# Kernel tuning notes

Measured on AMD Instinct MI355X. Metric: run time of the kernel, lower is better.

Reference implementation:

```python
import jax, jax.numpy as jnp
import numpy as np
import math

D_INNER = 512
D_STATE = 16
DT_RANK = 32
B_SZ = 2
L_SEQ = 4096


def setup_inputs() -> dict:
    key = jax.random.key(0)
    ks = jax.random.split(key, 6)
    x = jax.random.normal(ks[0], (B_SZ, L_SEQ, D_INNER), dtype=jnp.float32)
    # parameters (match torch init semantics closely enough for a numeric baseline)
    A = jnp.arange(1, D_STATE + 1, dtype=jnp.float32)
    A_log = jnp.broadcast_to(jnp.log(A)[None, :], (D_INNER, D_STATE)).copy()
    D_param = jnp.ones((D_INNER,), dtype=jnp.float32)
    # x_proj: Linear(d_inner -> dt_rank + 2*d_state), no bias
    W_xproj = jax.random.normal(ks[1], (DT_RANK + 2 * D_STATE, D_INNER), dtype=jnp.float32) / np.sqrt(D_INNER)
    # dt_proj: Linear(dt_rank -> d_inner) with special bias init
    W_dt = jax.random.normal(ks[2], (D_INNER, DT_RANK), dtype=jnp.float32) / np.sqrt(DT_RANK)
    dt_init = jnp.exp(jax.random.uniform(ks[3], (D_INNER,)) * (math.log(0.1) - math.log(0.001)) + math.log(0.001))
    b_dt = jnp.log(jnp.exp(dt_init) - 1.0)
    alpha = jnp.asarray(0.6, dtype=jnp.float32)
    beta_logit = jnp.asarray(math.log(0.99 / (1.0 - 0.99 + 1e-08)), dtype=jnp.float32)
    return {"x": x, "A_log": A_log, "D_param": D_param, "W_xproj": W_xproj,
            "W_dt": W_dt, "b_dt": b_dt, "alpha": alpha, "beta_logit": beta_logit}


def _momentum_ssm(x, A_log, D_param, W_xproj, W_dt, b_dt, alpha, beta_logit):
    # x: (B, L, D)
    proj = jnp.einsum('bld,pd->blp', x, W_xproj)            # (B, L, r+2N)
    dt_in = proj[..., :DT_RANK]
    Bp = proj[..., DT_RANK:DT_RANK + D_STATE]                # (B, L, N)
    Cp = proj[..., DT_RANK + D_STATE:]                       # (B, L, N)
    dt = jax.nn.softplus(jnp.einsum('blr,dr->bld', dt_in, W_dt) + b_dt)  # (B, L, D)
    A = -jnp.exp(A_log)                                      # (D, N)
    A_bar = jnp.exp(dt[..., None] * A[None, None])           # (B, L, D, N)
    # fused B_bar * x_t: dt * Bp * x
    inp = dt[..., None] * Bp[:, :, None, :] * x[..., None]   # (B, L, D, N)
    beta = jax.nn.sigmoid(beta_logit)

    # scan over time; carry (h, v): (B, D, N)
    h0 = jnp.zeros((x.shape[0], D_INNER, D_STATE), dtype=x.dtype)
    v0 = jnp.zeros_like(h0)

    def step(carry, ts):
        h, v = carry
        a_t, inp_t, c_t = ts                                 # (B,D,N), (B,D,N), (B,N)
        v = beta * v + alpha * inp_t
        h = a_t * h + v
        y = jnp.einsum('bdn,bn->bd', h, c_t)
        return (h, v), y

    xs = (jnp.moveaxis(A_bar, 1, 0), jnp.moveaxis(inp, 1, 0), jnp.moveaxis(Cp, 1, 0))
    _, ys = jax.lax.scan(step, (h0, v0), xs)                 # ys: (L, B, D)
    y = jnp.moveaxis(ys, 0, 1)                               # (B, L, D)
    return y + D_param * x


def reference(x, A_log, D_param, W_xproj, W_dt, b_dt, alpha, beta_logit):
    return _momentum_ssm(x, A_log, D_param, W_xproj, W_dt, b_dt, alpha, beta_logit)
```

## Files before the change

kernel.cpp:

```cpp
#include <hip/hip_runtime.h>


#define D_IN 512
#define D_ST 16
#define DTR  32
#define BSZ  2
#define LSEQ 4096
#define PDIM 64
#define NCH  256
#define LCH  (LSEQ / NCH)
#define LOG2E 1.44269504f
#define LN2   0.69314718f

typedef __attribute__((ext_vector_type(8))) short short8;
typedef __attribute__((ext_vector_type(4))) float f32x4;
typedef _Float16 f16;
typedef __attribute__((ext_vector_type(8))) _Float16 f16x8;

__device__ inline float fast_exp2(float x) { return __builtin_amdgcn_exp2f(x); }
__device__ inline float fast_log2(float x) { return __builtin_amdgcn_logf(x); }

__device__ inline unsigned short bf16_rne(float f) {
  unsigned b = __float_as_uint(f);
  return (unsigned short)((b + 0x7fffu + ((b >> 16) & 1u)) >> 16);
}

__device__ inline void cvt8(const float4 u, const float4 v, short8& hi, short8& lo) {
  float f[8] = {u.x, u.y, u.z, u.w, v.x, v.y, v.z, v.w};
#pragma unroll
  for (int i = 0; i < 8; ++i) {
    unsigned short h = bf16_rne(f[i]);
    hi[i] = (short)h;
    float r = f[i] - __uint_as_float((unsigned)h << 16);
    lo[i] = (short)bf16_rne(r);
  }
}

__device__ inline void st8h(f16* p, const float* s) {
  f16 t[8];
#pragma unroll
  for (int i = 0; i < 8; ++i) t[i] = (f16)s[i];
  *(f16x8*)p = *(f16x8*)&t[0];
}
__device__ inline void ld16h(const f16* p, float* d) {
  f16x8 a = *(const f16x8*)p;
  f16x8 b = *(const f16x8*)(p + 8);
#pragma unroll
  for (int i = 0; i < 8; ++i) { d[i] = (float)a[i]; d[8 + i] = (float)b[i]; }
}

__device__ inline bool loadA2(const float* A_log, int d, float* A2) {
  const float4* ap = (const float4*)(A_log + (size_t)d * D_ST);
#pragma unroll
  for (int i = 0; i < 4; ++i) {
    float4 a4 = ap[i];
    A2[4 * i + 0] = -__expf(a4.x) * LOG2E;
    A2[4 * i + 1] = -__expf(a4.y) * LOG2E;
    A2[4 * i + 2] = -__expf(a4.z) * LOG2E;
    A2[4 * i + 3] = -__expf(a4.w) * LOG2E;
  }
  bool pw = true;
#pragma unroll
  for (int n = 1; n < 16; ++n) {
    float ref = (float)(n + 1) * A2[0];
    pw = pw && (fabsf(A2[n] - ref) <= 2e-5f * fabsf(ref));
  }
  return pw;
}

__global__ __launch_bounds__(256) void k_wprep(const float* __restrict__ W,
                                               short* __restrict__ Whi,
                                               short* __restrict__ Wlo) {
  const int i = (blockIdx.x * 256 + threadIdx.x) * 4;
  float4 w = *(const float4*)(W + i);
  float f[4] = {w.x, w.y, w.z, w.w};
  unsigned short h[4], lo[4];
#pragma unroll
  for (int j = 0; j < 4; ++j) {
    h[j] = bf16_rne(f[j]);
    float r = f[j] - __uint_as_float((unsigned)h[j] << 16);
    lo[j] = bf16_rne(r);
  }
  *(uint2*)(Whi + i) = make_uint2(h[0] | ((unsigned)h[1] << 16), h[2] | ((unsigned)h[3] << 16));
  *(uint2*)(Wlo + i) = make_uint2(lo[0] | ((unsigned)lo[1] << 16), lo[2] | ((unsigned)lo[3] << 16));
}

#define MM3(ACC, AH, AL, BH, BL)                                        \
  ACC = __builtin_amdgcn_mfma_f32_16x16x32_bf16(AL, BH, ACC, 0, 0, 0);  \
  ACC = __builtin_amdgcn_mfma_f32_16x16x32_bf16(AH, BL, ACC, 0, 0, 0);  \
  ACC = __builtin_amdgcn_mfma_f32_16x16x32_bf16(AH, BH, ACC, 0, 0, 0);

#define LOADB(P, S)                                   \
  {                                                   \
    const int kb = ((S) & 15) * 32;                   \
    P##h0 = *(const short8*)(bh + kb);                \
    P##h1 = *(const short8*)(bh + 8192 + kb);         \
    P##h2 = *(const short8*)(bh + 16384 + kb);        \
    P##h3 = *(const short8*)(bh + 24576 + kb);        \
    P##l0 = *(const short8*)(bl + kb);                \
    P##l1 = *(const short8*)(bl + 8192 + kb);         \
    P##l2 = *(const short8*)(bl + 16384 + kb);        \
    P##l3 = *(const short8*)(bl + 24576 + kb);        \
  }

#define LOADA(Aa, Ab, S)                              \
  {                                                   \
    const int ka = ((S) & 15) * 32;                   \
    Aa = *(const float4*)(xr + ka);                   \
    Ab = *(const float4*)(xr + ka + 4);               \
  }

#define SUBSTEP(Aa, Ab, P, SA, SB)                    \
  {                                                   \
    short8 ahi, alo;                                  \
    cvt8(Aa, Ab, ahi, alo);                           \
    MM3(acc0, ahi, alo, P##h0, P##l0);                \
    MM3(acc1, ahi, alo, P##h1, P##l1);                \
    MM3(acc2, ahi, alo, P##h2, P##l2);                \
    MM3(acc3, ahi, alo, P##h3, P##l3);                \
    LOADB(P, SB);                                     \
    LOADA(Aa, Ab, SA);                                \
  }

__global__ __launch_bounds__(64) void k_proj(const float* __restrict__ x,
                                             const short* __restrict__ Whi,
                                             const short* __restrict__ Wlo,
                                             float* __restrict__ proj) {
  const int row0 = blockIdx.x * 16;
  const int l = threadIdx.x;
  const int m = l & 15;
  const int ko = (l >> 4) * 8;
  const float* xr = x + (size_t)(row0 + m) * D_IN + ko;
  const short* bh = Whi + (size_t)m * D_IN + ko;
  const short* bl = Wlo + (size_t)m * D_IN + ko;

  f32x4 acc0 = {0.f, 0.f, 0.f, 0.f}, acc1 = acc0, acc2 = acc0, acc3 = acc0;
  float4 A0a, A0b, A1a, A1b, A2a, A2b, A3a, A3b;
  short8 Xh0, Xh1, Xh2, Xh3, Xl0, Xl1, Xl2, Xl3;
  short8 Yh0, Yh1, Yh2, Yh3, Yl0, Yl1, Yl2, Yl3;
  LOADA(A0a, A0b, 0); LOADA(A1a, A1b, 1); LOADA(A2a, A2b, 2); LOADA(A3a, A3b, 3);
  LOADB(X, 0); LOADB(Y, 1);

#pragma unroll
  for (int it = 0; it < 4; ++it) {
    const int s = it * 4;
    SUBSTEP(A0a, A0b, X, s + 4, s + 2);
    SUBSTEP(A1a, A1b, Y, s + 5, s + 3);
    SUBSTEP(A2a, A2b, X, s + 6, s + 4);
    SUBSTEP(A3a, A3b, Y, s + 7, s + 5);
  }

  const int r0 = (l >> 4) * 4;
#pragma unroll
  for (int r = 0; r < 4; ++r) {
    float* pr = proj + (size_t)(row0 + r0 + r) * PDIM + m;
    pr[0] = acc0[r]; pr[16] = acc1[r]; pr[32] = acc2[r]; pr[48] = acc3[r];
  }
}


#define PWCHK(val, n)                                                        \
  pw = pw && (fabsf((val) - (float)((n) + 1) * a0) <=                        \
              2e-5f * fabsf((float)((n) + 1) * a0));

#define S1_LOOP                                                              \
  _Pragma("unroll")                                                          \
  for (int j = 0; j < LCH; ++j) {                                            \
    const float4* pj = (const float4*)&Ps[j][16 * hf];                       \
    float c0 = 0.f, c1 = 0.f, c2 = 0.f, c3 = 0.f;                            \
    _Pragma("unroll")                                                        \
    for (int k = 0; k < 4; ++k) {                                            \
      float4 p = pj[k];                                                      \
      c0 = fmaf(p.x, w4[k].x, c0);                                           \
      c1 = fmaf(p.y, w4[k].y, c1);                                           \
      c2 = fmaf(p.z, w4[k].z, c2);                                           \
      c3 = fmaf(p.w, w4[k].w, c3);                                           \
    }                                                                        \
    const float part = (c0 + c1) + (c2 + c3);                                \
    const float acc = part + __shfl_xor(part, 1, 64) + bb;                   \
    const float ee = fast_exp2(acc * LOG2E);                                 \
    const float dtc = (acc > 20.f) ? acc : LN2 * fast_log2(1.f + ee);        \
    if (hf == 0) dp[(size_t)j * D_IN] = (f16)dtc;                            \
    sd += dtc;                                                               \
    bpow *= beta;                                                            \
    const float xv = xs[j];                                                  \
    const float u = alpha * dtc * xv;                                        \
    float4 B0 = *(const float4*)&Ps[j][DTR + 8 * hf];                        \
    float4 B1 = *(const float4*)&Ps[j][DTR + 8 * hf + 4];                    \
    const float Bf[8] = {B0.x, B0.y, B0.z, B0.w, B1.x, B1.y, B1.z, B1.w};    \
    AR_INIT;                                                                 \
    _Pragma("unroll")                                                        \
    for (int k = 0; k < 8; ++k) {                                            \
      AR_STEP;                                                               \
      v8[k] = fmaf(beta, v8[k], u * Bf[k]);                                  \
      h8[k] = fmaf(ar, h8[k], v8[k]);                                        \
      cv8[k] = fmaf(ar, cv8[k], bpow);                                       \
    }                                                                        \
  }

__global__ __launch_bounds__(256) void k_scan1(const float* __restrict__ x,
                                               const float* __restrict__ proj,
                                               const float* __restrict__ A_log,
                                               const float* __restrict__ W_dt,
                                               const float* __restrict__ b_dt,
                                               const float* __restrict__ alpha_p,
                                               const float* __restrict__ beta_p,
                                               f16* __restrict__ hh,
                                               f16* __restrict__ vh,
                                               f16* __restrict__ cvv,
                                               float* __restrict__ sdt,
                                               f16* __restrict__ dth) {
  __shared__ float Ps[LCH][PDIM];
  const int c = blockIdx.x, b = blockIdx.z;
  const int hf = threadIdx.x & 1;
  const int d = blockIdx.y * 128 + (threadIdx.x >> 1);
  const int t0 = c * LCH;
  {
    const float4* src = (const float4*)(proj + ((size_t)b * LSEQ + t0) * PDIM);
    ((float4*)&Ps[0][0])[threadIdx.x] = src[threadIdx.x];
  }
  float xs[LCH];
  {
    const float* xp = x + ((size_t)b * LSEQ + t0) * D_IN + d;
#pragma unroll
    for (int j = 0; j < LCH; ++j) xs[j] = xp[(size_t)j * D_IN];
  }
  float4 w4[4];
  {
    const float4* wp = (const float4*)(W_dt + (size_t)d * DTR + 16 * hf);
#pragma unroll
    for (int i = 0; i < 4; ++i) w4[i] = wp[i];
  }
  const float bb = b_dt[d];
  const float alpha = alpha_p[0];
  const float beta = 1.f / (1.f + __expf(-beta_p[0]));

  float4 e0, e1, e2, e3;
  {
    const float4* ap = (const float4*)(A_log + (size_t)d * D_ST);
    float4 r0 = ap[0], r1 = ap[1], r2 = ap[2], r3 = ap[3];
    e0 = make_float4(-__expf(r0.x) * LOG2E, -__expf(r0.y) * LOG2E,
                     -__expf(r0.z) * LOG2E, -__expf(r0.w) * LOG2E);
    e1 = make_float4(-__expf(r1.x) * LOG2E, -__expf(r1.y) * LOG2E,
                     -__expf(r1.z) * LOG2E, -__expf(r1.w) * LOG2E);
    e2 = make_float4(-__expf(r2.x) * LOG2E, -__expf(r2.y) * LOG2E,
                     -__expf(r2.z) * LOG2E, -__expf(r2.w) * LOG2E);
    e3 = make_float4(-__expf(r3.x) * LOG2E, -__expf(r3.y) * LOG2E,
                     -__expf(r3.z) * LOG2E, -__expf(r3.w) * LOG2E);
  }
  const float a0 = e0.x;
  bool pw = true;
  PWCHK(e0.y, 1) PWCHK(e0.z, 2) PWCHK(e0.w, 3)
  PWCHK(e1.x, 4) PWCHK(e1.y, 5) PWCHK(e1.z, 6) PWCHK(e1.w, 7)
  PWCHK(e2.x, 8) PWCHK(e2.y, 9) PWCHK(e2.z, 10) PWCHK(e2.w, 11)
  PWCHK(e3.x, 12) PWCHK(e3.y, 13) PWCHK(e3.z, 14) PWCHK(e3.w, 15)
  float A2h[8];
  {
    float4 u0 = hf ? e2 : e0;
    float4 u1 = hf ? e3 : e1;
    A2h[0] = u0.x; A2h[1] = u0.y; A2h[2] = u0.z; A2h[3] = u0.w;
    A2h[4] = u1.x; A2h[5] = u1.y; A2h[6] = u1.z; A2h[7] = u1.w;
  }
  __syncthreads();

  f16* dp = dth + ((size_t)b * LSEQ + t0) * D_IN + d;
  float h8[8] = {}, v8[8] = {}, cv8[8] = {};
  float bpow = 1.f, sd = 0.f;

  if (pw) {
#define AR_INIT                                                   \
    const float r = fast_exp2(dtc * a0);                          \
    const float r2 = r * r;                                       \
    const float r4 = r2 * r2;                                     \
    float ar = hf ? r4 * r4 : 1.f
#define AR_STEP ar *= r
    S1_LOOP
#undef AR_INIT
#undef AR_STEP
  } else {
#define AR_INIT float ar
#define AR_STEP ar = fast_exp2(dtc * A2h[k])
    S1_LOOP
#undef AR_INIT
#undef AR_STEP
  }

  const size_t base = ((size_t)(b * NCH + c) * D_IN + d) * D_ST + hf * 8;
  st8h(hh + base, h8);
  st8h(vh + base, v8);
  st8h(cvv + base, cv8);
  if (hf == 0) sdt[(size_t)(b * NCH + c) * D_IN + d] = sd;
}

__global__ __launch_bounds__(64) void k_fix(f16* __restrict__ hh,
                                            f16* __restrict__ vh,
                                            const f16* __restrict__ cvv,
                                            const float* __restrict__ sdt,
                                            const float* __restrict__ A_log,
                                            const float* __restrict__ beta_p) {
  const int g = blockIdx.x * 64 + threadIdx.x;
  const int b = g >> 13;
  const int dn = g & 8191;
  const float beta = 1.f / (1.f + __expf(-beta_p[0]));
  const float A2 = -__expf(A_log[dn]) * LOG2E;
  float bL = beta;
#pragma unroll
  for (int i = 0; i < 4; ++i) bL *= bL;

  const size_t cs = (size_t)D_IN * D_ST;
  const size_t base = (size_t)b * NCH * cs + dn;
  const size_t sbase = (size_t)b * NCH * D_IN + (dn >> 4);

  float hg[8], vg[8], cg[8], sg[8];
#pragma unroll
  for (int i = 0; i < 8; ++i) {
    hg[i] = (float)hh[base + i * cs];
    vg[i] = (float)vh[base + i * cs];
    cg[i] = (float)cvv[base + i * cs];
    sg[i] = sdt[sbase + i * D_IN];
  }
  float H = 0.f, V = 0.f;
  for (int c0 = 0; c0 < NCH; c0 += 8) {
    const int cp = (c0 + 8) & (NCH - 1);
    float hn[8], vn[8], cn[8], sn[8];
#pragma unroll
    for (int i = 0; i < 8; ++i) {
      hn[i] = (float)hh[base + (size_t)(cp + i) * cs];
      vn[i] = (float)vh[base + (size_t)(cp + i) * cs];
      cn[i] = (float)cvv[base + (size_t)(cp + i) * cs];
      sn[i] = sdt[sbase + (size_t)(cp + i) * D_IN];
    }
#pragma unroll
    for (int i = 0; i < 8; ++i) {
      hh[base + (size_t)(c0 + i) * cs] = (f16)H;
      vh[base + (size_t)(c0 + i) * cs] = (f16)V;
      const float Pa = fast_exp2(sg[i] * A2);
      const float Hn = fmaf(Pa, H, fmaf(cg[i], V, hg[i]));
      V = fmaf(bL, V, vg[i]);
      H = Hn;
    }
#pragma unroll
    for (int i = 0; i < 8; ++i) { hg[i] = hn[i]; vg[i] = vn[i]; cg[i] = cn[i]; sg[i] = sn[i]; }
  }
}

#define S2_BODY(GET_A)                                        \
  _Pragma("unroll")                                           \
  for (int j = 0; j < LCH; ++j) {                             \
    const float dtc = dtv[j], xv = xs[j];                     \
    const float u = alpha * dtc * xv;                         \
    GET_A;                                                    \
    float4 Bq[8];                                             \
    _Pragma("unroll")                                         \
    for (int i = 0; i < 8; ++i) Bq[i] = ((const float4*)&Ps[j][DTR])[i]; \
    const float* Bf = (const float*)Bq;                       \
    float y0 = 0.f, y1 = 0.f, y2 = 0.f, y3 = 0.f;             \
    float ar = 1.f;                                           \
    _Pragma("unroll")                                         \
    for (int n = 0; n < 16; ++n) {                            \
      NEXT_A(ar, n);                                          \
      v[n] = fmaf(beta, v[n], u * Bf[n]);                     \
      h[n] = fmaf(ar, h[n], v[n]);                            \
      float hc = h[n] * Bf[16 + n];                           \
      if ((n & 3) == 0) y0 += hc;                             \
      else if ((n & 3) == 1) y1 += hc;                        \
      else if ((n & 3) == 2) y2 += hc;                        \
      else y3 += hc;                                          \
    }                                                         \
    op[(size_t)j * D_IN] = (y0 + y1) + (y2 + y3) + Dv * xv;   \
  }

__global__ __launch_bounds__(256) void k_scan2(const float* __restrict__ x,
                                               const f16* __restrict__ dth,
                                               const float* __restrict__ proj,
                                               const float* __restrict__ A_log,
                                               const float* __restrict__ D_param,
                                               const float* __restrict__ alpha_p,
                                               const float* __restrict__ beta_p,
                                               const f16* __restrict__ hh,
                                               const f16* __restrict__ vh,
                                               float* __restrict__ out) {
  __shared__ float Ps[LCH][PDIM];
  const int c = blockIdx.x, b = blockIdx.z;
  const int d = blockIdx.y * 256 + threadIdx.x;
  const int t0 = c * LCH;
  {
    const float4* src = (const float4*)(proj + ((size_t)b * LSEQ + t0) * PDIM);
    ((float4*)&Ps[0][0])[threadIdx.x] = src[threadIdx.x];
  }
  float xs[LCH], dtv[LCH];
  {
    const float* xp = x + ((size_t)b * LSEQ + t0) * D_IN + d;
    const f16* dp = dth + ((size_t)b * LSEQ + t0) * D_IN + d;
#pragma unroll
    for (int j = 0; j < LCH; ++j) xs[j] = xp[(size_t)j * D_IN];
#pragma unroll
    for (int j = 0; j < LCH; ++j) dtv[j] = (float)dp[(size_t)j * D_IN];
  }
  const float alpha = alpha_p[0];
  const float beta = 1.f / (1.f + __expf(-beta_p[0]));
  const float Dv = D_param[d];
  float A2[D_ST];
  const bool powA = loadA2(A_log, d, A2);
  const size_t ibase = ((size_t)(b * NCH + c) * D_IN + d) * D_ST;
  float h[16], v[16];
  ld16h(hh + ibase, h);
  ld16h(vh + ibase, v);
  __syncthreads();

  float* op = out + ((size_t)b * LSEQ + t0) * D_IN + d;
  if (powA) {
#define NEXT_A(ar, n) ar *= r
    S2_BODY(const float r = fast_exp2(dtc * A2[0]))
#undef NEXT_A
  } else {
#define NEXT_A(ar, n) ar = fast_exp2(dtc * A2[n])
    S2_BODY()
#undef NEXT_A
  }
}

extern "C" void kernel_launch(void* const* d_in, const int* in_sizes, int n_in,
                              void* d_out, int out_size, void* d_ws, size_t ws_size,
                              hipStream_t stream) {
  const float* x = (const float*)d_in[0];
  const float* A_log = (const float*)d_in[1];
  const float* D_param = (const float*)d_in[2];
  const float* W_xproj = (const float*)d_in[3];
  const float* W_dt = (const float*)d_in[4];
  const float* b_dt = (const float*)d_in[5];
  const float* alpha = (const float*)d_in[6];
  const float* beta_logit = (const float*)d_in[7];
  float* out = (float*)d_out;

  const size_t NST = (size_t)BSZ * NCH * D_IN * D_ST;
  float* ws = (float*)d_ws;
  float* proj = ws;
  float* sdt = proj + (size_t)BSZ * LSEQ * PDIM;
  f16* hh = (f16*)(sdt + (size_t)BSZ * NCH * D_IN);
  f16* vh = hh + NST;
  f16* cvv = vh + NST;
  f16* dth = cvv + NST;
  short* Whi = (short*)(dth + (size_t)BSZ * LSEQ * D_IN);
  short* Wlo = Whi + (size_t)PDIM * D_IN;

  k_wprep<<<dim3(PDIM * D_IN / 1024), dim3(256), 0, stream>>>(W_xproj, Whi, Wlo);
  k_proj<<<dim3(BSZ * LSEQ / 16), dim3(64), 0, stream>>>(x, Whi, Wlo, proj);
  k_scan1<<<dim3(NCH, D_IN / 128, BSZ), dim3(256), 0, stream>>>(
      x, proj, A_log, W_dt, b_dt, alpha, beta_logit, hh, vh, cvv, sdt, dth);
  k_fix<<<dim3(BSZ * D_IN * D_ST / 64), dim3(64), 0, stream>>>(hh, vh, cvv, sdt, A_log,
                                                               beta_logit);
  k_scan2<<<dim3(NCH, D_IN / 256, BSZ), dim3(256), 0, stream>>>(
      x, dth, proj, A_log, D_param, alpha, beta_logit, hh, vh, out);
}
```

Before: 176.0 us.

## Use one thread per channel in scan1 and read proj directly from global

The first scan kernel drops the two-threads-per-channel split (which needed a shuffle and half-state registers), so each thread now handles all 16 states and the full dt dot product. Both scan kernels stop staging proj rows through shared memory and a barrier, reading them straight from global memory, where all threads in a block share the same rows. The non-power fallback recomputes A on the fly through volatile loads instead of holding it in registers. Together this halves the scan1 grid and removes syncs, at the cost of more registers per thread and less parallelism.

```diff
diff --git a/kernel.cpp b/kernel.cpp
--- a/kernel.cpp
+++ b/kernel.cpp
@@ -36,11 +36,12 @@
   }
 }
 
-__device__ inline void st8h(f16* p, const float* s) {
-  f16 t[8];
-#pragma unroll
-  for (int i = 0; i < 8; ++i) t[i] = (f16)s[i];
+__device__ inline void st16h(f16* p, const float* s) {
+  f16 t[16];
+#pragma unroll
+  for (int i = 0; i < 16; ++i) t[i] = (f16)s[i];
   *(f16x8*)p = *(f16x8*)&t[0];
+  *(f16x8*)(p + 8) = *(f16x8*)&t[8];
 }
 __device__ inline void ld16h(const f16* p, float* d) {
   f16x8 a = *(const f16x8*)p;
@@ -49,22 +50,27 @@
   for (int i = 0; i < 8; ++i) { d[i] = (float)a[i]; d[8 + i] = (float)b[i]; }
 }
 
-__device__ inline bool loadA2(const float* A_log, int d, float* A2) {
+#define PWCHK(val, n)                                                        \
+  pw = pw && (fabsf((val) - (float)((n) + 1) * a0) <=                        \
+              2e-5f * fabsf((float)((n) + 1) * a0));
+
+__device__ inline bool detectA2(const float* __restrict__ A_log, int d, float& a0) {
   const float4* ap = (const float4*)(A_log + (size_t)d * D_ST);
-#pragma unroll
-  for (int i = 0; i < 4; ++i) {
-    float4 a4 = ap[i];
-    A2[4 * i + 0] = -__expf(a4.x) * LOG2E;
-    A2[4 * i + 1] = -__expf(a4.y) * LOG2E;
-    A2[4 * i + 2] = -__expf(a4.z) * LOG2E;
-    A2[4 * i + 3] = -__expf(a4.w) * LOG2E;
-  }
+  float4 r0 = ap[0], r1 = ap[1], r2 = ap[2], r3 = ap[3];
+  float4 e0 = make_float4(-__expf(r0.x) * LOG2E, -__expf(r0.y) * LOG2E,
+                          -__expf(r0.z) * LOG2E, -__expf(r0.w) * LOG2E);
+  float4 e1 = make_float4(-__expf(r1.x) * LOG2E, -__expf(r1.y) * LOG2E,
+                          -__expf(r1.z) * LOG2E, -__expf(r1.w) * LOG2E);
+  float4 e2 = make_float4(-__expf(r2.x) * LOG2E, -__expf(r2.y) * LOG2E,
+                          -__expf(r2.z) * LOG2E, -__expf(r2.w) * LOG2E);
+  float4 e3 = make_float4(-__expf(r3.x) * LOG2E, -__expf(r3.y) * LOG2E,
+                          -__expf(r3.z) * LOG2E, -__expf(r3.w) * LOG2E);
+  a0 = e0.x;
   bool pw = true;
-#pragma unroll
-  for (int n = 1; n < 16; ++n) {
-    float ref = (float)(n + 1) * A2[0];
-    pw = pw && (fabsf(A2[n] - ref) <= 2e-5f * fabsf(ref));
-  }
+  PWCHK(e0.y, 1) PWCHK(e0.z, 2) PWCHK(e0.w, 3)
+  PWCHK(e1.x, 4) PWCHK(e1.y, 5) PWCHK(e1.z, 6) PWCHK(e1.w, 7)
+  PWCHK(e2.x, 8) PWCHK(e2.y, 9) PWCHK(e2.z, 10) PWCHK(e2.w, 11)
+  PWCHK(e3.x, 12) PWCHK(e3.y, 13) PWCHK(e3.z, 14) PWCHK(e3.w, 15)
   return pw;
 }
 
@@ -158,43 +164,39 @@
   }
 }
 
-
-#define PWCHK(val, n)                                                        \
-  pw = pw && (fabsf((val) - (float)((n) + 1) * a0) <=                        \
-              2e-5f * fabsf((float)((n) + 1) * a0));
-
 #define S1_LOOP                                                              \
   _Pragma("unroll")                                                          \
   for (int j = 0; j < LCH; ++j) {                                            \
-    const float4* pj = (const float4*)&Ps[j][16 * hf];                       \
-    float c0 = 0.f, c1 = 0.f, c2 = 0.f, c3 = 0.f;                            \
-    _Pragma("unroll")                                                        \
-    for (int k = 0; k < 4; ++k) {                                            \
-      float4 p = pj[k];                                                      \
-      c0 = fmaf(p.x, w4[k].x, c0);                                           \
-      c1 = fmaf(p.y, w4[k].y, c1);                                           \
-      c2 = fmaf(p.z, w4[k].z, c2);                                           \
-      c3 = fmaf(p.w, w4[k].w, c3);                                           \
+    const float4* pj = (const float4*)(pb + j * PDIM);                       \
+    float4 pp[8];                                                            \
+    _Pragma("unroll")                                                        \
+    for (int k = 0; k < 8; ++k) pp[k] = pj[k];                               \
+    float c0 = bb, c1 = 0.f, c2 = 0.f, c3 = 0.f;                             \
+    _Pragma("unroll")                                                        \
+    for (int k = 0; k < 8; ++k) {                                            \
+      c0 = fmaf(pp[k].x, w4[k].x, c0);                                       \
+      c1 = fmaf(pp[k].y, w4[k].y, c1);                                       \
+      c2 = fmaf(pp[k].z, w4[k].z, c2);                                       \
+      c3 = fmaf(pp[k].w, w4[k].w, c3);                                       \
     }                                                                        \
-    const float part = (c0 + c1) + (c2 + c3);                                \
-    const float acc = part + __shfl_xor(part, 1, 64) + bb;                   \
+    const float acc = (c0 + c1) + (c2 + c3);                                 \
     const float ee = fast_exp2(acc * LOG2E);                                 \
     const float dtc = (acc > 20.f) ? acc : LN2 * fast_log2(1.f + ee);        \
-    if (hf == 0) dp[(size_t)j * D_IN] = (f16)dtc;                            \
+    dp[(size_t)j * D_IN] = (f16)dtc;                                         \
     sd += dtc;                                                               \
     bpow *= beta;                                                            \
-    const float xv = xs[j];                                                  \
-    const float u = alpha * dtc * xv;                                        \
-    float4 B0 = *(const float4*)&Ps[j][DTR + 8 * hf];                        \
-    float4 B1 = *(const float4*)&Ps[j][DTR + 8 * hf + 4];                    \
-    const float Bf[8] = {B0.x, B0.y, B0.z, B0.w, B1.x, B1.y, B1.z, B1.w};    \
+    const float u = alpha * dtc * xs[j];                                     \
+    float4 bq[4];                                                            \
+    _Pragma("unroll")                                                        \
+    for (int k = 0; k < 4; ++k) bq[k] = pj[8 + k];                           \
+    const float* Bf = (const float*)bq;                                      \
     AR_INIT;                                                                 \
     _Pragma("unroll")                                                        \
-    for (int k = 0; k < 8; ++k) {                                            \
+    for (int n = 0; n < 16; ++n) {                                           \
       AR_STEP;                                                               \
-      v8[k] = fmaf(beta, v8[k], u * Bf[k]);                                  \
-      h8[k] = fmaf(ar, h8[k], v8[k]);                                        \
-      cv8[k] = fmaf(ar, cv8[k], bpow);                                       \
+      v[n] = fmaf(beta, v[n], u * Bf[n]);                                    \
+      h[n] = fmaf(ar, h[n], v[n]);                                           \
+      cv[n] = fmaf(ar, cv[n], bpow);                                         \
     }                                                                        \
   }
 
@@ -210,86 +212,53 @@
                                                f16* __restrict__ cvv,
                                                float* __restrict__ sdt,
                                                f16* __restrict__ dth) {
-  __shared__ float Ps[LCH][PDIM];
   const int c = blockIdx.x, b = blockIdx.z;
-  const int hf = threadIdx.x & 1;
-  const int d = blockIdx.y * 128 + (threadIdx.x >> 1);
+  const int d = blockIdx.y * 256 + threadIdx.x;
   const int t0 = c * LCH;
-  {
-    const float4* src = (const float4*)(proj + ((size_t)b * LSEQ + t0) * PDIM);
-    ((float4*)&Ps[0][0])[threadIdx.x] = src[threadIdx.x];
-  }
+  const float* pb = proj + ((size_t)b * LSEQ + t0) * PDIM;
+
   float xs[LCH];
   {
     const float* xp = x + ((size_t)b * LSEQ + t0) * D_IN + d;
 #pragma unroll
     for (int j = 0; j < LCH; ++j) xs[j] = xp[(size_t)j * D_IN];
   }
-  float4 w4[4];
+  float4 w4[8];
   {
-    const float4* wp = (const float4*)(W_dt + (size_t)d * DTR + 16 * hf);
-#pragma unroll
-    for (int i = 0; i < 4; ++i) w4[i] = wp[i];
+    const float4* wp = (const float4*)(W_dt + (size_t)d * DTR);
+#pragma unroll
+    for (int i = 0; i < 8; ++i) w4[i] = wp[i];
   }
   const float bb = b_dt[d];
   const float alpha = alpha_p[0];
   const float beta = 1.f / (1.f + __expf(-beta_p[0]));
-
-  float4 e0, e1, e2, e3;
-  {
-    const float4* ap = (const float4*)(A_log + (size_t)d * D_ST);
-    float4 r0 = ap[0], r1 = ap[1], r2 = ap[2], r3 = ap[3];
-    e0 = make_float4(-__expf(r0.x) * LOG2E, -__expf(r0.y) * LOG2E,
-                     -__expf(r0.z) * LOG2E, -__expf(r0.w) * LOG2E);
-    e1 = make_float4(-__expf(r1.x) * LOG2E, -__expf(r1.y) * LOG2E,
-                     -__expf(r1.z) * LOG2E, -__expf(r1.w) * LOG2E);
-    e2 = make_float4(-__expf(r2.x) * LOG2E, -__expf(r2.y) * LOG2E,
-                     -__expf(r2.z) * LOG2E, -__expf(r2.w) * LOG2E);
-    e3 = make_float4(-__expf(r3.x) * LOG2E, -__expf(r3.y) * LOG2E,
-                     -__expf(r3.z) * LOG2E, -__expf(r3.w) * LOG2E);
-  }
-  const float a0 = e0.x;
-  bool pw = true;
-  PWCHK(e0.y, 1) PWCHK(e0.z, 2) PWCHK(e0.w, 3)
-  PWCHK(e1.x, 4) PWCHK(e1.y, 5) PWCHK(e1.z, 6) PWCHK(e1.w, 7)
-  PWCHK(e2.x, 8) PWCHK(e2.y, 9) PWCHK(e2.z, 10) PWCHK(e2.w, 11)
-  PWCHK(e3.x, 12) PWCHK(e3.y, 13) PWCHK(e3.z, 14) PWCHK(e3.w, 15)
-  float A2h[8];
-  {
-    float4 u0 = hf ? e2 : e0;
-    float4 u1 = hf ? e3 : e1;
-    A2h[0] = u0.x; A2h[1] = u0.y; A2h[2] = u0.z; A2h[3] = u0.w;
-    A2h[4] = u1.x; A2h[5] = u1.y; A2h[6] = u1.z; A2h[7] = u1.w;
-  }
-  __syncthreads();
+  float a0;
+  const bool pw = detectA2(A_log, d, a0);
 
   f16* dp = dth + ((size_t)b * LSEQ + t0) * D_IN + d;
-  float h8[8] = {}, v8[8] = {}, cv8[8] = {};
+  float h[16] = {}, v[16] = {}, cv[16] = {};
   float bpow = 1.f, sd = 0.f;
 
   if (pw) {
-#define AR_INIT                                                   \
-    const float r = fast_exp2(dtc * a0);                          \
-    const float r2 = r * r;                                       \
-    const float r4 = r2 * r2;                                     \
-    float ar = hf ? r4 * r4 : 1.f
+#define AR_INIT const float r = fast_exp2(dtc * a0); float ar = 1.f
 #define AR_STEP ar *= r
     S1_LOOP
 #undef AR_INIT
 #undef AR_STEP
   } else {
+    volatile const float* av = A_log + (size_t)d * D_ST;
 #define AR_INIT float ar
-#define AR_STEP ar = fast_exp2(dtc * A2h[k])
+#define AR_STEP ar = fast_exp2(dtc * (-__expf(av[n]) * LOG2E))
     S1_LOOP
 #undef AR_INIT
 #undef AR_STEP
   }
 
-  const size_t base = ((size_t)(b * NCH + c) * D_IN + d) * D_ST + hf * 8;
-  st8h(hh + base, h8);
-  st8h(vh + base, v8);
-  st8h(cvv + base, cv8);
-  if (hf == 0) sdt[(size_t)(b * NCH + c) * D_IN + d] = sd;
+  const size_t base = ((size_t)(b * NCH + c) * D_IN + d) * D_ST;
+  st16h(hh + base, h);
+  st16h(vh + base, v);
+  st16h(cvv + base, cv);
+  sdt[(size_t)(b * NCH + c) * D_IN + d] = sd;
 }
 
 __global__ __launch_bounds__(64) void k_fix(f16* __restrict__ hh,
@@ -344,30 +313,30 @@
   }
 }
 
-#define S2_BODY(GET_A)                                        \
-  _Pragma("unroll")                                           \
-  for (int j = 0; j < LCH; ++j) {                             \
-    const float dtc = dtv[j], xv = xs[j];                     \
-    const float u = alpha * dtc * xv;                         \
-    GET_A;                                                    \
-    float4 Bq[8];                                             \
-    _Pragma("unroll")                                         \
-    for (int i = 0; i < 8; ++i) Bq[i] = ((const float4*)&Ps[j][DTR])[i]; \
-    const float* Bf = (const float*)Bq;                       \
-    float y0 = 0.f, y1 = 0.f, y2 = 0.f, y3 = 0.f;             \
-    float ar = 1.f;                                           \
-    _Pragma("unroll")                                         \
-    for (int n = 0; n < 16; ++n) {                            \
-      NEXT_A(ar, n);                                          \
-      v[n] = fmaf(beta, v[n], u * Bf[n]);                     \
-      h[n] = fmaf(ar, h[n], v[n]);                            \
-      float hc = h[n] * Bf[16 + n];                           \
-      if ((n & 3) == 0) y0 += hc;                             \
-      else if ((n & 3) == 1) y1 += hc;                        \
-      else if ((n & 3) == 2) y2 += hc;                        \
-      else y3 += hc;                                          \
-    }                                                         \
-    op[(size_t)j * D_IN] = (y0 + y1) + (y2 + y3) + Dv * xv;   \
+#define S2_LOOP                                                              \
+  _Pragma("unroll")                                                          \
+  for (int j = 0; j < LCH; ++j) {                                            \
+    const float4* pj = (const float4*)(pb + j * PDIM);                       \
+    float4 bq[8];                                                            \
+    _Pragma("unroll")                                                        \
+    for (int k = 0; k < 8; ++k) bq[k] = pj[8 + k];                           \
+    const float* Bf = (const float*)bq;                                      \
+    const float dtc = dtv[j], xv = xs[j];                                    \
+    const float u = alpha * dtc * xv;                                        \
+    float y0 = 0.f, y1 = 0.f, y2 = 0.f, y3 = 0.f;                            \
+    AR_INIT;                                                                 \
+    _Pragma("unroll")                                                        \
+    for (int n = 0; n < 16; ++n) {                                           \
+      AR_STEP;                                                               \
+      v[n] = fmaf(beta, v[n], u * Bf[n]);                                    \
+      h[n] = fmaf(ar, h[n], v[n]);                                           \
+      float hc = h[n] * Bf[16 + n];                                          \
+      if ((n & 3) == 0) y0 += hc;                                            \
+      else if ((n & 3) == 1) y1 += hc;                                       \
+      else if ((n & 3) == 2) y2 += hc;                                       \
+      else y3 += hc;                                                         \
+    }                                                                        \
+    op[(size_t)j * D_IN] = (y0 + y1) + (y2 + y3) + Dv * xv;                  \
   }
 
 __global__ __launch_bounds__(256) void k_scan2(const float* __restrict__ x,
@@ -380,14 +349,11 @@
                                                const f16* __restrict__ hh,
                                                const f16* __restrict__ vh,
                                                float* __restrict__ out) {
-  __shared__ float Ps[LCH][PDIM];
   const int c = blockIdx.x, b = blockIdx.z;
   const int d = blockIdx.y * 256 + threadIdx.x;
   const int t0 = c * LCH;
-  {
-    const float4* src = (const float4*)(proj + ((size_t)b * LSEQ + t0) * PDIM);
-    ((float4*)&Ps[0][0])[threadIdx.x] = src[threadIdx.x];
-  }
+  const float* pb = proj + ((size_t)b * LSEQ + t0) * PDIM;
+
   float xs[LCH], dtv[LCH];
   {
     const float* xp = x + ((size_t)b * LSEQ + t0) * D_IN + d;
@@ -400,23 +366,27 @@
   const float alpha = alpha_p[0];
   const float beta = 1.f / (1.f + __expf(-beta_p[0]));
   const float Dv = D_param[d];
-  float A2[D_ST];
-  const bool powA = loadA2(A_log, d, A2);
+  float a0;
+  const bool pw = detectA2(A_log, d, a0);
   const size_t ibase = ((size_t)(b * NCH + c) * D_IN + d) * D_ST;
   float h[16], v[16];
   ld16h(hh + ibase, h);
   ld16h(vh + ibase, v);
-  __syncthreads();
 
   float* op = out + ((size_t)b * LSEQ + t0) * D_IN + d;
-  if (powA) {
-#define NEXT_A(ar, n) ar *= r
-    S2_BODY(const float r = fast_exp2(dtc * A2[0]))
-#undef NEXT_A
+  if (pw) {
+#define AR_INIT const float r = fast_exp2(dtc * a0); float ar = 1.f
+#define AR_STEP ar *= r
+    S2_LOOP
+#undef AR_INIT
+#undef AR_STEP
   } else {
-#define NEXT_A(ar, n) ar = fast_exp2(dtc * A2[n])
-    S2_BODY()
-#undef NEXT_A
+    volatile const float* av = A_log + (size_t)d * D_ST;
+#define AR_INIT float ar
+#define AR_STEP ar = fast_exp2(dtc * (-__expf(av[n]) * LOG2E))
+    S2_LOOP
+#undef AR_INIT
+#undef AR_STEP
   }
 }
 
@@ -446,7 +416,7 @@
 
   k_wprep<<<dim3(PDIM * D_IN / 1024), dim3(256), 0, stream>>>(W_xproj, Whi, Wlo);
   k_proj<<<dim3(BSZ * LSEQ / 16), dim3(64), 0, stream>>>(x, Whi, Wlo, proj);
-  k_scan1<<<dim3(NCH, D_IN / 128, BSZ), dim3(256), 0, stream>>>(
+  k_scan1<<<dim3(NCH, D_IN / 256, BSZ), dim3(256), 0, stream>>>(
       x, proj, A_log, W_dt, b_dt, alpha, beta_logit, hh, vh, cvv, sdt, dth);
   k_fix<<<dim3(BSZ * D_IN * D_ST / 64), dim3(64), 0, stream>>>(hh, vh, cvv, sdt, A_log,
                                                                beta_logit);
```

New measurement: 175.9 us. About the same (-0.1%).
